# Optimization experiments

Measured on AMD Instinct MI355X. Metric: run time of the kernel, lower is better.

Reference implementation:

```python
import jax, jax.numpy as jnp
import numpy as np

NUM_HEADS = 8

def setup_inputs() -> dict:
    key = jax.random.key(0)
    ks = jax.random.split(key, 9)
    b, s, d = 2, 2048, 512
    e = d * NUM_HEADS  # 4096
    sc = 0.02
    return {
        "x": jax.random.normal(ks[0], (b, s, d), jnp.float32),
        "Wq": jax.random.normal(ks[1], (e, d), jnp.float32) * sc,
        "bq": jax.random.normal(ks[2], (e,), jnp.float32) * sc,
        "Wk": jax.random.normal(ks[3], (e, d), jnp.float32) * sc,
        "bk": jax.random.normal(ks[4], (e,), jnp.float32) * sc,
        "Wv": jax.random.normal(ks[5], (e, d), jnp.float32) * sc,
        "bv": jax.random.normal(ks[6], (e,), jnp.float32) * sc,
        "Wo": jax.random.normal(ks[7], (d, e), jnp.float32) * sc,
        "bo": jax.random.normal(ks[8], (d,), jnp.float32) * sc,
    }

def reference(x, Wq, bq, Wk, bk, Wv, bv, Wo, bo):
    b, s, d = x.shape
    h = NUM_HEADS
    hd = d  # head_dim == model_dimension in this module
    # QKV projections: [b, s, h*hd]
    q = (x @ Wq.T + bq).reshape(b, s, h, hd)
    k = (x @ Wk.T + bk).reshape(b, s, h, hd)
    v = (x @ Wv.T + bv).reshape(b, s, h, hd)
    # scores: [b, h, s_q, s_k]
    scores = jnp.einsum("bqhd,bkhd->bhqk", q, k) / jnp.sqrt(jnp.float32(hd))
    attn = jax.nn.softmax(scores, axis=-1)
    ctx = jnp.einsum("bhqk,bkhd->bqhd", attn, v).reshape(b, s, h * hd)
    return ctx @ Wo.T + bo
```

## Files before the change

### kernel.cpp

```cpp
#include <hip/hip_runtime.h>
#include <hip/hip_bf16.h>

typedef __hip_bfloat16 bf16t;
typedef short bf16x8 __attribute__((ext_vector_type(8)));
typedef float f32x4 __attribute__((ext_vector_type(4)));

__device__ __forceinline__ float b2f(short s) {
    unsigned u = ((unsigned)(unsigned short)s) << 16;
    float f;
    __builtin_memcpy(&f, &u, 4);
    return f;
}

__device__ __forceinline__ unsigned short f2b(float f) {
    unsigned u;
    __builtin_memcpy(&u, &f, 4);
    unsigned r = (u + 0x7fffu + ((u >> 16) & 1u)) >> 16;
    return (unsigned short)r;
}

__device__ __forceinline__ void gload_lds16(const void* g, void* l) {
    __builtin_amdgcn_global_load_lds(
        (const __attribute__((address_space(1))) void*)g,
        (__attribute__((address_space(3))) void*)l,
        16, 0, 0);
}

template<int EPI>
__global__ __launch_bounds__(512, 2)
void gemm8p(const bf16t* __restrict__ Ag, const bf16t* __restrict__ Bg,
            void* __restrict__ Cg, const float* __restrict__ bias,
            float* __restrict__ part,
            int K, int lda, int ldb, int ldc,
            long aOffB, long aOffH, long bOffB, long bOffH,
            long cOffB, long cOffH, float scale)
{
    __shared__ __align__(16) char lds8[131072];

    unsigned gx = gridDim.x, gy = gridDim.y;
    unsigned nwg = gx * gy * gridDim.z;
    unsigned wg = (blockIdx.z * gy + blockIdx.y) * gx + blockIdx.x;
    if ((nwg & 7u) == 0u) wg = (wg & 7u) * (nwg >> 3) + (wg >> 3);
    const unsigned pz = wg / (gx * gy);
    const unsigned prem = wg - pz * gx * gy;
    const unsigned py = prem / gx;
    const unsigned px = prem - py * gx;

    const int zb = pz >> 3, zh = pz & 7;
    const int brow = py * 256;
    const int bcol = px * 256;

    const size_t ldab = (size_t)lda * 2;
    const size_t ldbb = (size_t)ldb * 2;
    const char* Agb = (const char*)(Ag + (size_t)zb * aOffB + (size_t)zh * aOffH)
                      + (size_t)brow * ldab;
    const char* Bgb = (const char*)(Bg + (size_t)zb * bOffB + (size_t)zh * bOffH)
                      + (size_t)bcol * ldbb;

    const int t    = threadIdx.x;
    const int lane = t & 63;
    const int wid  = t >> 6;
    const int wm   = wid >> 2;
    const int wn   = wid & 3;
    const int lr   = lane & 15;
    const int lk   = lane >> 4;

    const int srow = t >> 2;
    const int scg  = (t & 3) ^ ((srow >> 1) & 3);
    const size_t aSrc = (size_t)srow * ldab + (size_t)scg * 16;
    const size_t bSrc = (size_t)srow * ldbb + (size_t)scg * 16;
    const int dst0 = t * 16;
    char* ldsA = lds8;
    char* ldsB = lds8 + 65536;

    const int rchunk = lk ^ ((lr >> 1) & 3);
    const int aByte = (wm * 128 + lr) * 64 + rchunk * 16;
    const int bByte = (wn * 64 + lr) * 64 + rchunk * 16;

    f32x4 acc[8][4];
#pragma unroll
    for (int i = 0; i < 8; ++i)
#pragma unroll
        for (int j = 0; j < 4; ++j)
            acc[i][j] = (f32x4){0.f, 0.f, 0.f, 0.f};

    const int nk = K >> 5;

#define STAGE_A(kt, bufi) do {                                              \
        const char* s_ = Agb + (size_t)(kt) * 64 + aSrc;                    \
        char* d_ = ldsA + (bufi) * 16384 + dst0;                            \
        gload_lds16(s_, d_);                                                \
        gload_lds16(s_ + 128 * ldab, d_ + 8192);                            \
    } while (0)
#define STAGE_B(kt, bufi) do {                                              \
        const char* s_ = Bgb + (size_t)(kt) * 64 + bSrc;                    \
        char* d_ = ldsB + (bufi) * 16384 + dst0;                            \
        gload_lds16(s_, d_);                                                \
        gload_lds16(s_ + 128 * ldbb, d_ + 8192);                            \
    } while (0)

    const int npro = nk < 3 ? nk : 3;
    for (int p = 0; p < npro; ++p) { STAGE_A(p, p & 3); STAGE_B(p, p & 3); }
    if (npro == 3) asm volatile("s_waitcnt vmcnt(8)" ::: "memory");
    else           asm volatile("s_waitcnt vmcnt(0)" ::: "memory");
    __builtin_amdgcn_s_barrier();

    for (int kt = 0; kt < nk; ++kt) {
        const int buf  = kt & 3;
        const int bufS = (kt + 3) & 3;
        const bool st  = (kt + 3) < nk;
        const char* lA = ldsA + buf * 16384;
        const char* lB = ldsB + buf * 16384;

        bf16x8 af[4], bfv[4];
#pragma unroll
        for (int i = 0; i < 4; ++i) af[i]  = *(const bf16x8*)(lA + aByte + i * 1024);
#pragma unroll
        for (int j = 0; j < 4; ++j) bfv[j] = *(const bf16x8*)(lB + bByte + j * 1024);
        if (st) STAGE_A(kt + 3, bufS);
        __builtin_amdgcn_s_barrier();
        asm volatile("s_waitcnt lgkmcnt(0)" ::: "memory");
        __builtin_amdgcn_s_setprio(1);
#pragma unroll
        for (int i = 0; i < 4; ++i)
#pragma unroll
            for (int j = 0; j < 4; ++j)
                acc[i][j] = __builtin_amdgcn_mfma_f32_16x16x32_bf16(af[i], bfv[j], acc[i][j], 0, 0, 0);
        __builtin_amdgcn_s_setprio(0);
        asm volatile("" ::: "memory");
        __builtin_amdgcn_s_barrier();

        bf16x8 af2[4];
#pragma unroll
        for (int i = 0; i < 4; ++i) af2[i] = *(const bf16x8*)(lA + aByte + (i + 4) * 1024);
        if (st) STAGE_B(kt + 3, bufS);
        if (st)                  asm volatile("s_waitcnt vmcnt(8)" ::: "memory");
        else if (kt + 2 < nk)    asm volatile("s_waitcnt vmcnt(4)" ::: "memory");
        else if (kt + 1 < nk)    asm volatile("s_waitcnt vmcnt(0)" ::: "memory");
        __builtin_amdgcn_s_barrier();
        asm volatile("s_waitcnt lgkmcnt(0)" ::: "memory");
        __builtin_amdgcn_s_setprio(1);
#pragma unroll
        for (int i = 0; i < 4; ++i)
#pragma unroll
            for (int j = 0; j < 4; ++j)
                acc[i + 4][j] = __builtin_amdgcn_mfma_f32_16x16x32_bf16(af2[i], bfv[j], acc[i + 4][j], 0, 0, 0);
        __builtin_amdgcn_s_setprio(0);
        asm volatile("" ::: "memory");
        __builtin_amdgcn_s_barrier();
    }
#undef STAGE_A
#undef STAGE_B

    if (EPI == 4) {
#pragma unroll
        for (int i = 0; i < 8; ++i)
#pragma unroll
            for (int j = 0; j < 4; ++j)
#pragma unroll
                for (int r = 0; r < 4; ++r)
                    acc[i][j][r] = __expf(acc[i][j][r] * scale);
#pragma unroll
        for (int i = 0; i < 8; ++i)
#pragma unroll
            for (int r = 0; r < 4; ++r) {
                float v = acc[i][0][r] + acc[i][1][r] + acc[i][2][r] + acc[i][3][r];
                v += __shfl_xor(v, 1);
                v += __shfl_xor(v, 2);
                v += __shfl_xor(v, 4);
                v += __shfl_xor(v, 8);
                if (lr == 0)
                    part[((size_t)pz * 2048 + brow + wm * 128 + i * 16 + lk * 4 + r) * 32
                         + px * 4 + wn] = v;
            }
        __syncthreads();
        unsigned short* lC = (unsigned short*)lds8;
#pragma unroll
        for (int i = 0; i < 8; ++i)
#pragma unroll
            for (int j = 0; j < 4; ++j) {
                int col = wn * 64 + j * 16 + lr;
#pragma unroll
                for (int r = 0; r < 4; ++r) {
                    int row = wm * 128 + i * 16 + lk * 4 + r;
                    lC[row * 256 + col] = f2b(acc[i][j][r]);
                }
            }
        __syncthreads();
        unsigned short* C = (unsigned short*)((bf16t*)Cg + (size_t)zb * cOffB + (size_t)zh * cOffH);
#pragma unroll
        for (int p = 0; p < 16; ++p) {
            int c  = p * 512 + t;
            int row = c >> 5;
            int cc  = c & 31;
            bf16x8 v = *(const bf16x8*)(lC + (size_t)c * 8);
            *(bf16x8*)(C + (size_t)(brow + row) * ldc + bcol + cc * 8) = v;
        }
    } else if (EPI == 3) {
        __syncthreads();
        float* ldsInv = (float*)lds8;
        if (t < 256) {
            const float* pp = part + ((size_t)pz * 2048 + brow + t) * 32;
            float s = 0.f;
#pragma unroll
            for (int p = 0; p < 32; ++p) s += pp[p];
            ldsInv[t] = 1.0f / s;
        }
        __syncthreads();
        float linv[8][4];
#pragma unroll
        for (int i = 0; i < 8; ++i)
#pragma unroll
            for (int r = 0; r < 4; ++r)
                linv[i][r] = ldsInv[wm * 128 + i * 16 + lk * 4 + r];
        __syncthreads();
        unsigned short* lC = (unsigned short*)lds8;
#pragma unroll
        for (int i = 0; i < 8; ++i)
#pragma unroll
            for (int j = 0; j < 4; ++j) {
                int col = wn * 64 + j * 16 + lr;
#pragma unroll
                for (int r = 0; r < 4; ++r) {
                    int row = wm * 128 + i * 16 + lk * 4 + r;
                    lC[row * 256 + col] = f2b(acc[i][j][r] * linv[i][r]);
                }
            }
        __syncthreads();
        unsigned short* C = (unsigned short*)((bf16t*)Cg + (size_t)zb * cOffB + (size_t)zh * cOffH);
#pragma unroll
        for (int p = 0; p < 16; ++p) {
            int c  = p * 512 + t;
            int row = c >> 5;
            int cc  = c & 31;
            bf16x8 v = *(const bf16x8*)(lC + (size_t)c * 8);
            *(bf16x8*)(C + (size_t)(brow + row) * ldc + bcol + cc * 8) = v;
        }
    } else if (EPI == 5) {
        const int sel = bcol >> 12;
        const int colw0 = bcol & 4095;
        if (sel < 2) {
            __syncthreads();
            unsigned short* lC = (unsigned short*)lds8;
#pragma unroll
            for (int i = 0; i < 8; ++i)
#pragma unroll
                for (int j = 0; j < 4; ++j) {
                    int col = wn * 64 + j * 16 + lr;
                    float badd = bias[bcol + col];
#pragma unroll
                    for (int r = 0; r < 4; ++r) {
                        int row = wm * 128 + i * 16 + lk * 4 + r;
                        lC[row * 256 + col] = f2b(acc[i][j][r] + badd);
                    }
                }
            __syncthreads();
            unsigned short* C = (unsigned short*)((bf16t*)Cg + (size_t)sel * cOffB);
#pragma unroll
            for (int p = 0; p < 16; ++p) {
                int c  = p * 512 + t;
                int row = c >> 5;
                int cc  = c & 31;
                bf16x8 v = *(const bf16x8*)(lC + (size_t)c * 8);
                *(bf16x8*)(C + (size_t)(brow + row) * ldc + colw0 + cc * 8) = v;
            }
        } else {
            unsigned short* C = (unsigned short*)part;
#pragma unroll
            for (int i = 0; i < 8; ++i)
#pragma unroll
                for (int j = 0; j < 4; ++j) {
                    int col = colw0 + wn * 64 + j * 16 + lr;
                    int hh = col >> 9, dd = col & 511;
                    float badd = bias[8192 + col];
                    int row0 = brow + wm * 128 + i * 16 + lk * 4;
                    int bb = row0 >> 11, ss0 = row0 & 2047;
                    ushort4 pack;
                    pack.x = f2b(acc[i][j][0] + badd);
                    pack.y = f2b(acc[i][j][1] + badd);
                    pack.z = f2b(acc[i][j][2] + badd);
                    pack.w = f2b(acc[i][j][3] + badd);
                    size_t addr = ((((size_t)(bb * 8 + hh)) * 512 + dd) << 11) + (size_t)ss0;
                    *(ushort4*)(C + addr) = pack;
                }
        }
    } else {
        unsigned short* C = (unsigned short*)Cg;
#pragma unroll
        for (int i = 0; i < 8; ++i)
#pragma unroll
            for (int j = 0; j < 4; ++j) {
                int col = bcol + wn * 64 + j * 16 + lr;
                int hh = col >> 9, dd = col & 511;
                float badd = bias ? bias[col] : 0.f;
                int row0 = brow + wm * 128 + i * 16 + lk * 4;
                int bb = row0 >> 11, ss0 = row0 & 2047;
                ushort4 pack;
                pack.x = f2b(acc[i][j][0] * scale + badd);
                pack.y = f2b(acc[i][j][1] * scale + badd);
                pack.z = f2b(acc[i][j][2] * scale + badd);
                pack.w = f2b(acc[i][j][3] * scale + badd);
                size_t addr = ((((size_t)(bb * 8 + hh)) * 512 + dd) << 11) + (size_t)ss0;
                *(ushort4*)(C + addr) = pack;
            }
    }
}

__global__ __launch_bounds__(256, 3)
void gemm_of32(const bf16t* __restrict__ Ag, const bf16t* __restrict__ Bg,
               float* __restrict__ Cg, const float* __restrict__ bias,
               int K, int lda, int ldb, int ldc)
{
    __shared__ __align__(16) char lds[49152];

    unsigned gx = gridDim.x, gy = gridDim.y;
    unsigned nwg = gx * gy;
    unsigned wg = blockIdx.y * gx + blockIdx.x;
    if ((nwg & 7u) == 0u) wg = (wg & 7u) * (nwg >> 3) + (wg >> 3);
    const unsigned py = wg / gx;
    const unsigned px = wg - py * gx;
    const int brow = py * 128;
    const int bcol = px * 64;

    const int t    = threadIdx.x;
    const int lane = t & 63;
    const int wid  = t >> 6;
    const int wr   = wid >> 1, wc = wid & 1;
    const int lr   = lane & 15;
    const int lk   = lane >> 4;

    const size_t ldab = (size_t)lda * 2;
    const size_t ldbb = (size_t)ldb * 2;
    const char* Agb = (const char*)Ag + (size_t)brow * ldab;
    const char* Bgb = (const char*)Bg + (size_t)bcol * ldbb;

    const int srow = t >> 2;
    const int scg  = (t & 3) ^ ((srow >> 1) & 3);
    const size_t aSrc = (size_t)srow * ldab + (size_t)scg * 16;
    const size_t bSrc = (size_t)srow * ldbb + (size_t)scg * 16;
    char* ldsA = lds;
    char* ldsB = lds + 32768;

    const int rchunk = lk ^ ((lr >> 1) & 3);
    const int aByte = (wr * 64 + lr) * 64 + rchunk * 16;
    const int bByte = (wc * 32 + lr) * 64 + rchunk * 16;

    f32x4 acc[4][2];
#pragma unroll
    for (int i = 0; i < 4; ++i)
#pragma unroll
        for (int j = 0; j < 2; ++j)
            acc[i][j] = (f32x4){0.f, 0.f, 0.f, 0.f};

    const int nk = K >> 5;

#define STAGE_O(kt, bufi) do {                                              \
        const char* sa_ = Agb + (size_t)(kt) * 64 + aSrc;                   \
        gload_lds16(sa_,             ldsA + (bufi) * 8192 + t * 16);        \
        gload_lds16(sa_ + 64 * ldab, ldsA + (bufi) * 8192 + 4096 + t * 16); \
        gload_lds16(Bgb + (size_t)(kt) * 64 + bSrc,                         \
                    ldsB + (bufi) * 4096 + t * 16);                         \
    } while (0)

    for (int p = 0; p < 3; ++p) STAGE_O(p, p);
    asm volatile("s_waitcnt vmcnt(6)" ::: "memory");
    __builtin_amdgcn_s_barrier();

    for (int kt = 0; kt < nk; ++kt) {
        const int buf  = kt & 3;
        const bool st  = (kt + 3) < nk;
        const char* lA = ldsA + buf * 8192;
        const char* lB = ldsB + buf * 4096;

        bf16x8 af[4], bfv[2];
#pragma unroll
        for (int i = 0; i < 4; ++i) af[i]  = *(const bf16x8*)(lA + aByte + i * 1024);
#pragma unroll
        for (int j = 0; j < 2; ++j) bfv[j] = *(const bf16x8*)(lB + bByte + j * 1024);
        if (st) STAGE_O(kt + 3, (kt + 3) & 3);
        if (st)                  asm volatile("s_waitcnt vmcnt(6)" ::: "memory");
        else if (kt + 2 < nk)    asm volatile("s_waitcnt vmcnt(3)" ::: "memory");
        else if (kt + 1 < nk)    asm volatile("s_waitcnt vmcnt(0)" ::: "memory");
        __builtin_amdgcn_s_barrier();
        asm volatile("s_waitcnt lgkmcnt(0)" ::: "memory");
        __builtin_amdgcn_s_setprio(1);
#pragma unroll
        for (int i = 0; i < 4; ++i)
#pragma unroll
            for (int j = 0; j < 2; ++j)
                acc[i][j] = __builtin_amdgcn_mfma_f32_16x16x32_bf16(af[i], bfv[j], acc[i][j], 0, 0, 0);
        __builtin_amdgcn_s_setprio(0);
        asm volatile("" ::: "memory");
        __builtin_amdgcn_s_barrier();
    }
#undef STAGE_O

    const int orow = brow + wr * 64;
    const int ocol = bcol + wc * 32;
#pragma unroll
    for (int i = 0; i < 4; ++i)
#pragma unroll
        for (int j = 0; j < 2; ++j) {
            int col = ocol + j * 16 + lr;
            float badd = bias[col];
#pragma unroll
            for (int r = 0; r < 4; ++r) {
                int row = orow + i * 16 + lk * 4 + r;
                Cg[(size_t)row * ldc + col] = acc[i][j][r] + badd;
            }
        }
}

__global__ __launch_bounds__(256)
void cvt6(const float* __restrict__ s0, const float* __restrict__ s1,
          const float* __restrict__ s2, const float* __restrict__ s3,
          const float* __restrict__ s4,
          bf16t* __restrict__ d0, bf16t* __restrict__ d1,
          bf16t* __restrict__ d2, bf16t* __restrict__ d3,
          bf16t* __restrict__ d4,
          const float* __restrict__ bq, const float* __restrict__ bk,
          const float* __restrict__ bv, float* __restrict__ bqkv)
{
    int i = blockIdx.x * 256 + threadIdx.x;
    if (blockIdx.y == 5) {
        if (i < 3072) {
            int e = i * 4;
            const float* src = (e < 4096) ? (bq + e) : (e < 8192) ? (bk + e - 4096) : (bv + e - 8192);
            float4 f = *(const float4*)src;
            *(float4*)(bqkv + e) = f;
        }
        return;
    }
    const float* s;
    bf16t* d;
    switch (blockIdx.y) {
        case 0: s = s0; d = d0; break;
        case 1: s = s1; d = d1; break;
        case 2: s = s2; d = d2; break;
        case 3: s = s3; d = d3; break;
        default: s = s4; d = d4; break;
    }
    float4 f = ((const float4*)s)[i];
    ushort4 o;
    o.x = f2b(f.x); o.y = f2b(f.y); o.z = f2b(f.z); o.w = f2b(f.w);
    ((ushort4*)d)[i] = o;
}

extern "C" void kernel_launch(void* const* d_in, const int* in_sizes, int n_in,
                              void* d_out, int out_size, void* d_ws, size_t ws_size,
                              hipStream_t stream)
{
    const float* x  = (const float*)d_in[0];
    const float* Wq = (const float*)d_in[1];
    const float* bq = (const float*)d_in[2];
    const float* Wk = (const float*)d_in[3];
    const float* bk = (const float*)d_in[4];
    const float* Wv = (const float*)d_in[5];
    const float* bv = (const float*)d_in[6];
    const float* Wo = (const float*)d_in[7];
    const float* bo = (const float*)d_in[8];

    const int Bn = 2, Sn = 2048, Dn = 512, Hn = 8, En = 4096;
    const int Mn = Bn * Sn;
    const float scl = 0.044194173824159216f;

    bf16t* base = (bf16t*)d_ws;
    size_t off = 0;
    bf16t* Qb  = base + off; off += (size_t)Mn * En;
    bf16t* Kb  = base + off; off += (size_t)Mn * En;
    bf16t* Vt  = base + off; off += (size_t)Mn * En;
    bf16t* Xb  = base + off; off += (size_t)Mn * Dn;
    bf16t* Wc  = base + off; off += (size_t)3 * En * Dn;
    bf16t* Wob = base + off; off += (size_t)Dn * En;
    float* Pbias = (float*)(base + off); off += 12288;
    float* Pt  = (float*)(base + off); off += (size_t)16 * Sn * 32 * 2;
    bf16t* Sb  = base + off;

    cvt6<<<dim3(2048, 6, 1), 256, 0, stream>>>(
        x, Wq, Wk, Wv, Wo,
        Xb, Wc, Wc + (size_t)En * Dn, Wc + (size_t)2 * En * Dn, Wob,
        bq, bk, bv, Pbias);

    gemm8p<5><<<dim3(3 * En / 256, Mn / 256, 1), 512, 0, stream>>>(
        Xb, Wc, Qb, Pbias, (float*)Vt, Dn, Dn, Dn, En,
        0, 0, 0, 0, (long)Mn * En, 0, 1.0f);

    gemm8p<4><<<dim3(Sn / 256, Sn / 256, 16), 512, 0, stream>>>(
        Qb, Kb, Sb, nullptr, Pt, Dn, En, En, Sn,
        (long)Sn * En, (long)Dn, (long)Sn * En, (long)Dn,
        (long)Hn * Sn * Sn, (long)Sn * Sn, scl);

    gemm8p<3><<<dim3(Dn / 256, Sn / 256, 16), 512, 0, stream>>>(
        Sb, Vt, Qb, nullptr, Pt, Sn, Sn, Sn, En,
        (long)Hn * Sn * Sn, (long)Sn * Sn, (long)Hn * Dn * Sn, (long)Dn * Sn,
        (long)Sn * En, (long)Dn, 1.0f);

    gemm_of32<<<dim3(Dn / 64, Mn / 128, 1), 256, 0, stream>>>(
        Qb, Wob, (float*)d_out, bo, En, En, En, Dn);
}
```

Measured before the change: 303.7 us.

## Compute softmax row sums inside PV GEMM via ones-vector MFMA

The QK^T epilogue no longer computes row partial sums of exp scores with shuffles and global writes. A new dedicated PV kernel instead accumulates the row sum with an extra MFMA against a ones vector and normalises in its epilogue. The new kernel uses 128-row by full-512-column tiles, so each block reads its E tile only once, with triple buffering and a single block per CU. This removes the partial-sum buffer and its reduction, but the sum is now taken over bf16-rounded exps and the large LDS footprint limits occupancy.

```diff
diff --git a/kernel.cpp b/kernel.cpp
--- a/kernel.cpp
+++ b/kernel.cpp
@@ -4,13 +4,6 @@
 typedef __hip_bfloat16 bf16t;
 typedef short bf16x8 __attribute__((ext_vector_type(8)));
 typedef float f32x4 __attribute__((ext_vector_type(4)));
-
-__device__ __forceinline__ float b2f(short s) {
-    unsigned u = ((unsigned)(unsigned short)s) << 16;
-    float f;
-    __builtin_memcpy(&f, &u, 4);
-    return f;
-}
 
 __device__ __forceinline__ unsigned short f2b(float f) {
     unsigned u;
@@ -153,26 +146,6 @@
 #undef STAGE_B
 
     if (EPI == 4) {
-#pragma unroll
-        for (int i = 0; i < 8; ++i)
-#pragma unroll
-            for (int j = 0; j < 4; ++j)
-#pragma unroll
-                for (int r = 0; r < 4; ++r)
-                    acc[i][j][r] = __expf(acc[i][j][r] * scale);
-#pragma unroll
-        for (int i = 0; i < 8; ++i)
-#pragma unroll
-            for (int r = 0; r < 4; ++r) {
-                float v = acc[i][0][r] + acc[i][1][r] + acc[i][2][r] + acc[i][3][r];
-                v += __shfl_xor(v, 1);
-                v += __shfl_xor(v, 2);
-                v += __shfl_xor(v, 4);
-                v += __shfl_xor(v, 8);
-                if (lr == 0)
-                    part[((size_t)pz * 2048 + brow + wm * 128 + i * 16 + lk * 4 + r) * 32
-                         + px * 4 + wn] = v;
-            }
         __syncthreads();
         unsigned short* lC = (unsigned short*)lds8;
 #pragma unroll
@@ -183,7 +156,7 @@
 #pragma unroll
                 for (int r = 0; r < 4; ++r) {
                     int row = wm * 128 + i * 16 + lk * 4 + r;
-                    lC[row * 256 + col] = f2b(acc[i][j][r]);
+                    lC[row * 256 + col] = f2b(__expf(acc[i][j][r] * scale));
                 }
             }
         __syncthreads();
@@ -196,47 +169,7 @@
             bf16x8 v = *(const bf16x8*)(lC + (size_t)c * 8);
             *(bf16x8*)(C + (size_t)(brow + row) * ldc + bcol + cc * 8) = v;
         }
-    } else if (EPI == 3) {
-        __syncthreads();
-        float* ldsInv = (float*)lds8;
-        if (t < 256) {
-            const float* pp = part + ((size_t)pz * 2048 + brow + t) * 32;
-            float s = 0.f;
-#pragma unroll
-            for (int p = 0; p < 32; ++p) s += pp[p];
-            ldsInv[t] = 1.0f / s;
-        }
-        __syncthreads();
-        float linv[8][4];
-#pragma unroll
-        for (int i = 0; i < 8; ++i)
-#pragma unroll
-            for (int r = 0; r < 4; ++r)
-                linv[i][r] = ldsInv[wm * 128 + i * 16 + lk * 4 + r];
-        __syncthreads();
-        unsigned short* lC = (unsigned short*)lds8;
-#pragma unroll
-        for (int i = 0; i < 8; ++i)
-#pragma unroll
-            for (int j = 0; j < 4; ++j) {
-                int col = wn * 64 + j * 16 + lr;
-#pragma unroll
-                for (int r = 0; r < 4; ++r) {
-                    int row = wm * 128 + i * 16 + lk * 4 + r;
-                    lC[row * 256 + col] = f2b(acc[i][j][r] * linv[i][r]);
-                }
-            }
-        __syncthreads();
-        unsigned short* C = (unsigned short*)((bf16t*)Cg + (size_t)zb * cOffB + (size_t)zh * cOffH);
-#pragma unroll
-        for (int p = 0; p < 16; ++p) {
-            int c  = p * 512 + t;
-            int row = c >> 5;
-            int cc  = c & 31;
-            bf16x8 v = *(const bf16x8*)(lC + (size_t)c * 8);
-            *(bf16x8*)(C + (size_t)(brow + row) * ldc + bcol + cc * 8) = v;
-        }
-    } else if (EPI == 5) {
+    } else {
         const int sel = bcol >> 12;
         const int colw0 = bcol & 4095;
         if (sel < 2) {
@@ -284,25 +217,145 @@
                     *(ushort4*)(C + addr) = pack;
                 }
         }
-    } else {
-        unsigned short* C = (unsigned short*)Cg;
-#pragma unroll
-        for (int i = 0; i < 8; ++i)
-#pragma unroll
-            for (int j = 0; j < 4; ++j) {
-                int col = bcol + wn * 64 + j * 16 + lr;
-                int hh = col >> 9, dd = col & 511;
-                float badd = bias ? bias[col] : 0.f;
-                int row0 = brow + wm * 128 + i * 16 + lk * 4;
-                int bb = row0 >> 11, ss0 = row0 & 2047;
-                ushort4 pack;
-                pack.x = f2b(acc[i][j][0] * scale + badd);
-                pack.y = f2b(acc[i][j][1] * scale + badd);
-                pack.z = f2b(acc[i][j][2] * scale + badd);
-                pack.w = f2b(acc[i][j][3] * scale + badd);
-                size_t addr = ((((size_t)(bb * 8 + hh)) * 512 + dd) << 11) + (size_t)ss0;
-                *(ushort4*)(C + addr) = pack;
-            }
+    }
+}
+
+__global__ __launch_bounds__(512, 1)
+void gemm_pv(const bf16t* __restrict__ Eg, const bf16t* __restrict__ Vg,
+             bf16t* __restrict__ Cg)
+{
+    __shared__ __align__(16) char lds[122880];
+
+    unsigned wg = blockIdx.x;
+    wg = (wg & 7u) * 32u + (wg >> 3);
+    const int pz = wg >> 4;
+    const int py = wg & 15;
+    const int zb = pz >> 3, zh = pz & 7;
+    const int brow = py * 128;
+
+    const char* Agb = (const char*)Eg + ((size_t)pz * 2048 * 2048 + (size_t)brow * 2048) * 2;
+    const char* Bgb = (const char*)Vg + ((size_t)pz * 512 * 2048) * 2;
+
+    const int t    = threadIdx.x;
+    const int lane = t & 63;
+    const int wid  = t >> 6;
+    const int wm   = wid >> 2;
+    const int wn   = wid & 3;
+    const int lr   = lane & 15;
+    const int lk   = lane >> 4;
+
+    const int srow = t >> 2;
+    const int scg  = (t & 3) ^ ((srow >> 1) & 3);
+    const size_t aSrc = (size_t)srow * 4096 + (size_t)scg * 16;
+    const size_t bSrc = (size_t)srow * 4096 + (size_t)scg * 16;
+    char* ldsA = lds;
+    char* ldsB = lds + 24576;
+
+    const int rchunk = lk ^ ((lr >> 1) & 3);
+    const int aByte = (wm * 64 + lr) * 64 + rchunk * 16;
+    const int bByte = (wn * 128 + lr) * 64 + rchunk * 16;
+
+    f32x4 acc[4][8];
+#pragma unroll
+    for (int i = 0; i < 4; ++i)
+#pragma unroll
+        for (int j = 0; j < 8; ++j)
+            acc[i][j] = (f32x4){0.f, 0.f, 0.f, 0.f};
+    f32x4 accS[4];
+#pragma unroll
+    for (int i = 0; i < 4; ++i) accS[i] = (f32x4){0.f, 0.f, 0.f, 0.f};
+
+    bf16x8 ones;
+#pragma unroll
+    for (int e = 0; e < 8; ++e) ones[e] = (short)0x3F80;
+
+#define STAGE_PV(kt, bufi) do {                                             \
+        const char* sa_ = Agb + (size_t)(kt) * 64 + aSrc;                   \
+        gload_lds16(sa_, ldsA + (bufi) * 8192 + t * 16);                    \
+        const char* sb_ = Bgb + (size_t)(kt) * 64 + bSrc;                   \
+        char* db_ = ldsB + (bufi) * 32768 + t * 16;                         \
+        gload_lds16(sb_,               db_);                                \
+        gload_lds16(sb_ + 128 * 4096,  db_ + 8192);                         \
+        gload_lds16(sb_ + 256 * 4096,  db_ + 16384);                        \
+        gload_lds16(sb_ + 384 * 4096,  db_ + 24576);                        \
+    } while (0)
+
+    const int nk = 64;
+    STAGE_PV(0, 0);
+    STAGE_PV(1, 1);
+    asm volatile("s_waitcnt vmcnt(5)" ::: "memory");
+    __builtin_amdgcn_s_barrier();
+
+    int bufR = 0, bufS = 2;
+    for (int kt = 0; kt < nk; ++kt) {
+        const char* lA = ldsA + bufR * 8192;
+        const char* lB = ldsB + bufR * 32768;
+
+        bf16x8 af[4], bfv[8];
+#pragma unroll
+        for (int i = 0; i < 4; ++i) af[i]  = *(const bf16x8*)(lA + aByte + i * 1024);
+#pragma unroll
+        for (int j = 0; j < 8; ++j) bfv[j] = *(const bf16x8*)(lB + bByte + j * 1024);
+
+        if (kt + 2 < nk) {
+            STAGE_PV(kt + 2, bufS);
+            asm volatile("s_waitcnt vmcnt(5)" ::: "memory");
+        } else if (kt + 1 < nk) {
+            asm volatile("s_waitcnt vmcnt(0)" ::: "memory");
+        }
+        __builtin_amdgcn_s_barrier();
+        asm volatile("s_waitcnt lgkmcnt(0)" ::: "memory");
+        __builtin_amdgcn_s_setprio(1);
+#pragma unroll
+        for (int i = 0; i < 4; ++i) {
+            accS[i] = __builtin_amdgcn_mfma_f32_16x16x32_bf16(af[i], ones, accS[i], 0, 0, 0);
+#pragma unroll
+            for (int j = 0; j < 8; ++j)
+                acc[i][j] = __builtin_amdgcn_mfma_f32_16x16x32_bf16(af[i], bfv[j], acc[i][j], 0, 0, 0);
+        }
+        __builtin_amdgcn_s_setprio(0);
+        asm volatile("" ::: "memory");
+        __builtin_amdgcn_s_barrier();
+
+        bufR = (bufR == 2) ? 0 : bufR + 1;
+        bufS = (bufS == 2) ? 0 : bufS + 1;
+    }
+#undef STAGE_PV
+
+    float inv_[4][4];
+#pragma unroll
+    for (int i = 0; i < 4; ++i)
+#pragma unroll
+        for (int r = 0; r < 4; ++r)
+            inv_[i][r] = 1.0f / accS[i][r];
+
+    unsigned short* lC = (unsigned short*)lds;
+    unsigned short* C = (unsigned short*)(Cg + (size_t)zb * 2048 * 4096 + (size_t)zh * 512);
+#pragma unroll
+    for (int m = 0; m < 2; ++m) {
+        __syncthreads();
+        if (wm == m) {
+#pragma unroll
+            for (int i = 0; i < 4; ++i)
+#pragma unroll
+                for (int j = 0; j < 8; ++j) {
+                    int col = wn * 128 + j * 16 + lr;
+#pragma unroll
+                    for (int r = 0; r < 4; ++r) {
+                        int row = i * 16 + lk * 4 + r;
+                        lC[row * 512 + col] = f2b(acc[i][j][r] * inv_[i][r]);
+                    }
+                }
+        }
+        __syncthreads();
+#pragma unroll
+        for (int p = 0; p < 8; ++p) {
+            int c  = p * 512 + t;
+            int row = c >> 6;
+            int cc  = c & 63;
+            bf16x8 v = *(const bf16x8*)(lC + (size_t)c * 8);
+            *(bf16x8*)(C + (size_t)(brow + m * 64 + row) * 4096 + cc * 8) = v;
+        }
     }
 }
 
@@ -473,7 +526,6 @@
     bf16t* Wc  = base + off; off += (size_t)3 * En * Dn;
     bf16t* Wob = base + off; off += (size_t)Dn * En;
     float* Pbias = (float*)(base + off); off += 12288;
-    float* Pt  = (float*)(base + off); off += (size_t)16 * Sn * 32 * 2;
     bf16t* Sb  = base + off;
 
     cvt6<<<dim3(2048, 6, 1), 256, 0, stream>>>(
@@ -486,14 +538,11 @@
         0, 0, 0, 0, (long)Mn * En, 0, 1.0f);
 
     gemm8p<4><<<dim3(Sn / 256, Sn / 256, 16), 512, 0, stream>>>(
-        Qb, Kb, Sb, nullptr, Pt, Dn, En, En, Sn,
+        Qb, Kb, Sb, nullptr, nullptr, Dn, En, En, Sn,
         (long)Sn * En, (long)Dn, (long)Sn * En, (long)Dn,
         (long)Hn * Sn * Sn, (long)Sn * Sn, scl);
 
-    gemm8p<3><<<dim3(Dn / 256, Sn / 256, 16), 512, 0, stream>>>(
-        Sb, Vt, Qb, nullptr, Pt, Sn, Sn, Sn, En,
-        (long)Hn * Sn * Sn, (long)Sn * Sn, (long)Hn * Dn * Sn, (long)Dn * Sn,
-        (long)Sn * En, (long)Dn, 1.0f);
+    gemm_pv<<<256, 512, 0, stream>>>(Sb, Vt, Qb);
 
     gemm_of32<<<dim3(Dn / 64, Mn / 128, 1), 256, 0, stream>>>(
         Qb, Wob, (float*)d_out, bo, En, En, En, Dn);
```

Result: no change. 299.9 us (-1.3%).
